# Optimization experiments

Hardware: AMD Instinct MI355X
Metric: run time of the kernel (lower is better)

The kernel has to match this reference:

```python
import jax, jax.numpy as jnp
import numpy as np

T, B, D, H = 512, 64, 1024, 1024


def setup_inputs() -> dict:
    key = jax.random.key(0)
    ks = jax.random.split(key, 8)
    s_ih = 1.0 / np.sqrt(H)
    return {
        "inputs": jax.random.normal(ks[0], (T, B, D), dtype=jnp.float32),
        "h0": jax.random.normal(ks[1], (B, H), dtype=jnp.float32),
        "c0": jax.random.normal(ks[2], (B, H), dtype=jnp.float32),
        "W_ih": jax.random.uniform(ks[3], (4 * H, D), minval=-s_ih, maxval=s_ih, dtype=jnp.float32),
        "W_hh": jax.random.uniform(ks[4], (4 * H, H), minval=-s_ih, maxval=s_ih, dtype=jnp.float32),
        "b_ih": jax.random.uniform(ks[5], (4 * H,), minval=-s_ih, maxval=s_ih, dtype=jnp.float32),
        "b_hh": jax.random.uniform(ks[6], (4 * H,), minval=-s_ih, maxval=s_ih, dtype=jnp.float32),
    }


def _lstm_cell(x, h, c, W_ih, W_hh, b_ih, b_hh):
    # gates: [B, 4H] -> chunks (i, f, g, o), matching torch.nn.LSTMCell
    gates = x @ W_ih.T + b_ih + h @ W_hh.T + b_hh
    i, f, g, o = jnp.split(gates, 4, axis=-1)
    i = jax.nn.sigmoid(i)
    f = jax.nn.sigmoid(f)
    g = jnp.tanh(g)
    o = jax.nn.sigmoid(o)
    c_new = f * c + i * g
    h_new = o * jnp.tanh(c_new)
    return h_new, c_new


def reference(inputs, h0, c0, W_ih, W_hh, b_ih, b_hh):
    def step(carry, x_t):
        h, c = carry
        h, c = _lstm_cell(x_t, h, c, W_ih, W_hh, b_ih, b_hh)
        return (h, c), h

    (h_T, c_T), outputs = jax.lax.scan(step, (h0, c0), inputs)
    # outputs: [T, B, H] stacked per-timestep cell outputs
    return outputs, h_T, c_T
```

## Files before the change

### kernel.cpp

```cpp
#include <hip/hip_runtime.h>

#define T_STEPS 512
#define BATCH   64
#define DIM     1024
#define HID     1024
#define G4      4096
#define KTOT    2048
#define NKS     64

typedef __attribute__((ext_vector_type(8))) short s8v;
typedef __attribute__((ext_vector_type(4))) float f32x4;

__device__ __forceinline__ unsigned short f2bf(float f) {
    unsigned int u = __float_as_uint(f);
    u = u + 0x7FFFu + ((u >> 16) & 1u);
    return (unsigned short)(u >> 16);
}
__device__ __forceinline__ float bf2f(unsigned short s) {
    return __uint_as_float(((unsigned int)s) << 16);
}


__global__ __launch_bounds__(256) void pack_x(
    const float* __restrict__ inp, unsigned short* __restrict__ hi,
    unsigned short* __restrict__ lo)
{
    const size_t tau = (size_t)blockIdx.x * 256 + threadIdx.x;
    const int l  = (int)(tau & 63);
    const int m  = (int)((tau >> 6) & 3);
    const int ks = (int)((tau >> 8) & 31);
    const int t  = (int)(tau >> 13);
    const int b  = 16 * m + (l & 15);
    const int k  = ks * 32 + (l >> 4) * 8;
    const float* src = inp + ((size_t)t * BATCH + b) * DIM + k;
    float f[8];
    *(float4*)&f[0] = *(const float4*)src;
    *(float4*)&f[4] = *(const float4*)(src + 4);
    s8v vh, vl;
#pragma unroll
    for (int e = 0; e < 8; ++e) {
        const unsigned short h8 = f2bf(f[e]);
        vh[e] = (short)h8;
        vl[e] = (short)f2bf(f[e] - bf2f(h8));
    }
    *(s8v*)(hi + tau * 8) = vh;
    *(s8v*)(lo + tau * 8) = vl;
}

__global__ __launch_bounds__(256) void pack_w(
    const float* __restrict__ Wih, const float* __restrict__ Whh,
    unsigned short* __restrict__ hi, unsigned short* __restrict__ lo)
{
    const size_t tau = (size_t)blockIdx.x * 256 + threadIdx.x;
    const int l   = (int)(tau & 63);
    const int ks  = (int)((tau >> 6) & 63);
    const int bid = (int)(tau >> 12);
    const int c   = l & 15;
    const int n   = (c >> 2) * HID + bid * 4 + (c & 3);
    const int k   = ks * 32 + (l >> 4) * 8;
    const float* src = (k < DIM) ? (Wih + (size_t)n * DIM + k)
                                 : (Whh + (size_t)n * HID + (k - DIM));
    float f[8];
    *(float4*)&f[0] = *(const float4*)src;
    *(float4*)&f[4] = *(const float4*)(src + 4);
    s8v vh, vl;
#pragma unroll
    for (int e = 0; e < 8; ++e) {
        const unsigned short h8 = f2bf(f[e]);
        vh[e] = (short)h8;
        vl[e] = (short)f2bf(f[e] - bf2f(h8));
    }
    *(s8v*)(hi + tau * 8) = vh;
    *(s8v*)(lo + tau * 8) = vl;
}

__global__ __launch_bounds__(256) void pack_h0(
    const float* __restrict__ h0, unsigned short* __restrict__ hi,
    unsigned short* __restrict__ lo)
{
    const size_t tau = (size_t)blockIdx.x * 256 + threadIdx.x;
    const int l  = (int)(tau & 63);
    const int m  = (int)((tau >> 6) & 3);
    const int ks = (int)(tau >> 8);
    const int b  = 16 * m + (l & 15);
    const int j  = ks * 32 + (l >> 4) * 8;
    const float* src = h0 + (size_t)b * HID + j;
    float f[8];
    *(float4*)&f[0] = *(const float4*)src;
    *(float4*)&f[4] = *(const float4*)(src + 4);
    s8v vh, vl;
#pragma unroll
    for (int e = 0; e < 8; ++e) {
        const unsigned short h8 = f2bf(f[e]);
        vh[e] = (short)h8;
        vl[e] = (short)f2bf(f[e] - bf2f(h8));
    }
    *(s8v*)(hi + tau * 8) = vh;
    *(s8v*)(lo + tau * 8) = vl;
}

__global__ __launch_bounds__(512) void lstm_step_mfma(
    int t,
    const unsigned short* __restrict__ xPHi, const unsigned short* __restrict__ xPLo,
    const unsigned short* __restrict__ wPHi, const unsigned short* __restrict__ wPLo,
    const unsigned short* __restrict__ hPHi, const unsigned short* __restrict__ hPLo,
    unsigned short* __restrict__ hPHiW,      unsigned short* __restrict__ hPLoW,
    const float* __restrict__ cprev,
    const float* __restrict__ bih, const float* __restrict__ bhh,
    float* __restrict__ cbuf, float* __restrict__ out, float* __restrict__ tailp)
{
    __shared__ float part_s[8][64][8];
    __shared__ float gates_s[64][17];

    const int bid = blockIdx.x;
    const int tid = threadIdx.x;
    const int wv  = __builtin_amdgcn_readfirstlane(tid >> 6);
    const int l   = tid & 63;
    const int mg  = wv >> 2;
    const int kh  = wv & 3;
    const int par = t & 1;
    const int m0  = 2 * mg, m1 = 2 * mg + 1;

    const unsigned short *aHi, *aLo;
    if (kh < 2) {
        const size_t base = (((size_t)t * 32 + kh * 16) * 4) * 512;
        aHi = xPHi + base;  aLo = xPLo + base;
    } else {
        const size_t base = (((size_t)par * 32 + (kh - 2) * 16) * 4) * 512;
        aHi = hPHi + base;  aLo = hPLo + base;
    }
    const unsigned short* bHiP = wPHi + ((size_t)bid * 64 + kh * 16) * 512;
    const unsigned short* bLoP = wPLo + ((size_t)bid * 64 + kh * 16) * 512;

#define LDA(P, i, m) (*(const s8v*)((P) + ((size_t)(i) * 2048 + (m) * 512 + l * 8)))
#define LDB(P, i)    (*(const s8v*)((P) + ((size_t)(i) * 512 + l * 8)))

    f32x4 acc0 = {0.f, 0.f, 0.f, 0.f};
    f32x4 acc1 = {0.f, 0.f, 0.f, 0.f};

    s8v A0h = LDA(aHi, 0, m0), A0l = LDA(aLo, 0, m0);
    s8v A1h = LDA(aHi, 0, m1), A1l = LDA(aLo, 0, m1);
    s8v Bh  = LDB(bHiP, 0),    Bl  = LDB(bLoP, 0);

#pragma unroll 4
    for (int i = 0; i < 16; ++i) {
        s8v nA0h, nA0l, nA1h, nA1l, nBh, nBl;
        if (i < 15) {
            nA0h = LDA(aHi, i + 1, m0); nA0l = LDA(aLo, i + 1, m0);
            nA1h = LDA(aHi, i + 1, m1); nA1l = LDA(aLo, i + 1, m1);
            nBh  = LDB(bHiP, i + 1);    nBl  = LDB(bLoP, i + 1);
        }
        acc0 = __builtin_amdgcn_mfma_f32_16x16x32_bf16(A0h, Bh, acc0, 0, 0, 0);
        acc1 = __builtin_amdgcn_mfma_f32_16x16x32_bf16(A1h, Bh, acc1, 0, 0, 0);
        acc0 = __builtin_amdgcn_mfma_f32_16x16x32_bf16(A0h, Bl, acc0, 0, 0, 0);
        acc1 = __builtin_amdgcn_mfma_f32_16x16x32_bf16(A1h, Bl, acc1, 0, 0, 0);
        acc0 = __builtin_amdgcn_mfma_f32_16x16x32_bf16(A0l, Bh, acc0, 0, 0, 0);
        acc1 = __builtin_amdgcn_mfma_f32_16x16x32_bf16(A1l, Bh, acc1, 0, 0, 0);
        A0h = nA0h; A0l = nA0l; A1h = nA1h; A1l = nA1l; Bh = nBh; Bl = nBl;
    }
#undef LDA
#undef LDB

    *(f32x4*)&part_s[wv][l][0] = acc0;
    *(f32x4*)&part_s[wv][l][4] = acc1;
    __syncthreads();
    if (tid < 128) {
        const int mg2 = tid >> 6, l2 = tid & 63;
        f32x4 s0 = {0.f, 0.f, 0.f, 0.f};
        f32x4 s1 = {0.f, 0.f, 0.f, 0.f};
#pragma unroll
        for (int k = 0; k < 4; ++k) {
            s0 += *(const f32x4*)&part_s[mg2 * 4 + k][l2][0];
            s1 += *(const f32x4*)&part_s[mg2 * 4 + k][l2][4];
        }
        const int c = l2 & 15, rb = (l2 >> 4) * 4;
#pragma unroll
        for (int r = 0; r < 4; ++r) {
            gates_s[16 * (2 * mg2 + 0) + rb + r][c] = s0[r];
            gates_s[16 * (2 * mg2 + 1) + rb + r][c] = s1[r];
        }
    }
    __syncthreads();

    if (tid < 256) {
        const int b  = tid >> 2;
        const int jj = tid & 3;
        const int j  = bid * 4 + jj;
        const float pre_i = gates_s[b][0  + jj] + bih[0 * HID + j] + bhh[0 * HID + j];
        const float pre_f = gates_s[b][4  + jj] + bih[1 * HID + j] + bhh[1 * HID + j];
        const float pre_g = gates_s[b][8  + jj] + bih[2 * HID + j] + bhh[2 * HID + j];
        const float pre_o = gates_s[b][12 + jj] + bih[3 * HID + j] + bhh[3 * HID + j];
        const float ig = 1.0f / (1.0f + __expf(-pre_i));
        const float fg = 1.0f / (1.0f + __expf(-pre_f));
        const float gg = tanhf(pre_g);
        const float og = 1.0f / (1.0f + __expf(-pre_o));
        const float cp = cprev[b * HID + j];
        const float cn = fg * cp + ig * gg;
        const float hn = og * tanhf(cn);
        cbuf[b * HID + j] = cn;
        out[((size_t)t * BATCH + b) * HID + j] = hn;
        if (t == T_STEPS - 1) {
            tailp[b * HID + j] = hn;
            tailp[(size_t)BATCH * HID + b * HID + j] = cn;
        }
        const int parn = par ^ 1;
        const unsigned short hhi = f2bf(hn);
        const unsigned short hlo = f2bf(hn - bf2f(hhi));
        const size_t idx = ((((size_t)parn * 32 + (j >> 5)) * 4 + (b >> 4)) * 64
                            + ((b & 15) + 16 * ((j & 31) >> 3))) * 8 + (j & 7);
        hPHiW[idx] = hhi;
        hPLoW[idx] = hlo;
    }
}

__global__ __launch_bounds__(512) void lstm_step_f32(
    const float* __restrict__ x, const float* __restrict__ hprev,
    const float* __restrict__ cprev,
    const float* __restrict__ Wih, const float* __restrict__ Whh,
    const float* __restrict__ bih, const float* __restrict__ bhh,
    float* __restrict__ cnext, float* __restrict__ hout,
    float* __restrict__ tail)
{
    __shared__ float h_s[8][16][68];
    __shared__ float w_s[8][16][20];
    __shared__ float gates_s[64][17];
    float* part_s = &h_s[0][0][0];

    const int bid = blockIdx.x;
    const int tid = threadIdx.x;
    const int j0  = bid * 4;
    const int wv  = tid >> 6;
    const int gl  = tid & 63;
    const int b0  = (gl >> 2) * 4;
    const int c0_ = (gl & 3) * 4;

    const float* __restrict__ src = (wv < 4) ? x   : hprev;
    const float* __restrict__ W   = (wv < 4) ? Wih : Whh;
    const int kbase = (wv & 3) * 256;

    float acc[4][4] = {};
    float4 hv[4], wvf;

#pragma unroll
    for (int r = 0; r < 4; ++r) {
        const int fidx = r * 64 + gl;
        hv[r] = *(const float4*)(src + (fidx >> 2) * DIM + kbase + (fidx & 3) * 4);
    }
    {
        const int c = gl >> 2, k4 = (gl & 3) * 4;
        const int n = (c >> 2) * HID + j0 + (c & 3);
        wvf = *(const float4*)(W + (size_t)n * DIM + kbase + k4);
    }

    for (int ci = 0; ci < 16; ++ci) {
#pragma unroll
        for (int r = 0; r < 4; ++r) {
            const int fidx = r * 64 + gl;
            const int b = fidx >> 2, k4 = (fidx & 3) * 4;
            h_s[wv][k4 + 0][b] = hv[r].x; h_s[wv][k4 + 1][b] = hv[r].y;
            h_s[wv][k4 + 2][b] = hv[r].z; h_s[wv][k4 + 3][b] = hv[r].w;
        }
        {
            const int c = gl >> 2, k4 = (gl & 3) * 4;
            w_s[wv][k4 + 0][c] = wvf.x; w_s[wv][k4 + 1][c] = wvf.y;
            w_s[wv][k4 + 2][c] = wvf.z; w_s[wv][k4 + 3][c] = wvf.w;
        }
        if (ci < 15) {
            const int kb = kbase + (ci + 1) * 16;
#pragma unroll
            for (int r = 0; r < 4; ++r) {
                const int fidx = r * 64 + gl;
                hv[r] = *(const float4*)(src + (fidx >> 2) * DIM + kb + (fidx & 3) * 4);
            }
            {
                const int c = gl >> 2, k4 = (gl & 3) * 4;
                const int n = (c >> 2) * HID + j0 + (c & 3);
                wvf = *(const float4*)(W + (size_t)n * DIM + kb + k4);
            }
        }
#pragma unroll
        for (int kk = 0; kk < 16; ++kk) {
            const float4 h4 = *(const float4*)&h_s[wv][kk][b0];
            const float4 w4 = *(const float4*)&w_s[wv][kk][c0_];
            const float hr[4] = {h4.x, h4.y, h4.z, h4.w};
            const float wr[4] = {w4.x, w4.y, w4.z, w4.w};
#pragma unroll
            for (int i = 0; i < 4; ++i)
#pragma unroll
                for (int j = 0; j < 4; ++j)
                    acc[i][j] += hr[i] * wr[j];
        }
    }

    __syncthreads();
#pragma unroll
    for (int i = 0; i < 4; ++i)
#pragma unroll
        for (int j = 0; j < 4; ++j)
            part_s[tid * 17 + i * 4 + j] = acc[i][j];
    __syncthreads();
    if (tid < 64) {
#pragma unroll
        for (int i = 0; i < 4; ++i)
#pragma unroll
            for (int j = 0; j < 4; ++j) {
                const int idx = i * 4 + j;
                float s = 0.0f;
#pragma unroll
                for (int p = 0; p < 8; ++p)
                    s += part_s[(gl + 64 * p) * 17 + idx];
                gates_s[b0 + i][c0_ + j] = s;
            }
    }
    __syncthreads();

    if (tid < 256) {
        const int b  = tid >> 2;
        const int jj = tid & 3;
        const int j  = j0 + jj;
        const float pre_i = gates_s[b][0  + jj] + bih[0 * HID + j] + bhh[0 * HID + j];
        const float pre_f = gates_s[b][4  + jj] + bih[1 * HID + j] + bhh[1 * HID + j];
        const float pre_g = gates_s[b][8  + jj] + bih[2 * HID + j] + bhh[2 * HID + j];
        const float pre_o = gates_s[b][12 + jj] + bih[3 * HID + j] + bhh[3 * HID + j];
        const float ig = 1.0f / (1.0f + __expf(-pre_i));
        const float fg = 1.0f / (1.0f + __expf(-pre_f));
        const float gg = tanhf(pre_g);
        const float og = 1.0f / (1.0f + __expf(-pre_o));
        const float cp = cprev[b * HID + j];
        const float cn = fg * cp + ig * gg;
        const float hn = og * tanhf(cn);
        cnext[b * HID + j] = cn;
        hout[b * HID + j]  = hn;
        if (tail) {
            tail[b * HID + j] = hn;
            tail[(size_t)BATCH * HID + b * HID + j] = cn;
        }
    }
}

extern "C" void kernel_launch(void* const* d_in, const int* in_sizes, int n_in,
                              void* d_out, int out_size, void* d_ws, size_t ws_size,
                              hipStream_t stream) {
    const float* inputs = (const float*)d_in[0];
    const float* h0     = (const float*)d_in[1];
    const float* c0     = (const float*)d_in[2];
    const float* W_ih   = (const float*)d_in[3];
    const float* W_hh   = (const float*)d_in[4];
    const float* b_ih   = (const float*)d_in[5];
    const float* b_hh   = (const float*)d_in[6];
    float* out = (float*)d_out;

    const size_t XP = (size_t)T_STEPS * 32 * 4 * 512;
    const size_t WP = (size_t)256 * 64 * 512;
    const size_t HP = (size_t)2 * 32 * 4 * 512;
    const size_t needB = (2 * XP + 2 * WP + 2 * HP) * sizeof(unsigned short)
                         + (size_t)BATCH * HID * sizeof(float);

    if (ws_size >= needB) {
        unsigned short* xPHi = (unsigned short*)d_ws;
        unsigned short* xPLo = xPHi + XP;
        unsigned short* wPHi = xPLo + XP;
        unsigned short* wPLo = wPHi + WP;
        unsigned short* hPHi = wPLo + WP;
        unsigned short* hPLo = hPHi + HP;
        float* cbuf = (float*)(hPLo + HP);

        pack_x<<<dim3(16384), dim3(256), 0, stream>>>(inputs, xPHi, xPLo);
        pack_w<<<dim3(4096),  dim3(256), 0, stream>>>(W_ih, W_hh, wPHi, wPLo);
        pack_h0<<<dim3(32),   dim3(256), 0, stream>>>(h0, hPHi, hPLo);

        for (int t = 0; t < T_STEPS; ++t) {
            const float* cp = (t == 0) ? c0 : cbuf;
            float* tailp = out + (size_t)T_STEPS * BATCH * HID;
            lstm_step_mfma<<<dim3(256), dim3(512), 0, stream>>>(
                t, xPHi, xPLo, wPHi, wPLo, hPHi, hPLo, hPHi, hPLo,
                cp, b_ih, b_hh, cbuf, out, tailp);
        }
    } else {
        float* cbuf = (float*)d_ws;
        for (int t = 0; t < T_STEPS; ++t) {
            const float* x  = inputs + (size_t)t * BATCH * DIM;
            const float* hp = (t == 0) ? h0 : out + (size_t)(t - 1) * BATCH * HID;
            const float* cp = (t == 0) ? c0 : cbuf;
            float* ho   = out + (size_t)t * BATCH * HID;
            float* tailp = (t == T_STEPS - 1)
                         ? out + (size_t)T_STEPS * BATCH * HID : nullptr;
            lstm_step_f32<<<dim3(256), dim3(512), 0, stream>>>(
                x, hp, cp, W_ih, W_hh, b_ih, b_hh, cbuf, ho, tailp);
        }
    }
}
```

Baseline: 7.613 ms.

## Hoist input projection out of recurrence into chunked batched GEMM kernel

Moves the x@W_ih^T part of the gate computation out of the per-step kernel into a separate xproj_chunk kernel. That kernel computes the projection (plus both biases) for 64 timesteps at once and writes the results to a float buffer. The per-step kernel now only reduces over the hidden dimension, halving its serial K-loop, and reads the precomputed projection in its epilogue. The pack_x pre-pass is removed and splitting x into hi/lo bf16 is done inline, at the cost of an extra fp32 buffer round trip and an extra launch per chunk.

```diff
diff --git a/kernel.cpp b/kernel.cpp
--- a/kernel.cpp
+++ b/kernel.cpp
@@ -5,8 +5,7 @@
 #define DIM     1024
 #define HID     1024
 #define G4      4096
-#define KTOT    2048
-#define NKS     64
+#define TCH     64
 
 typedef __attribute__((ext_vector_type(8))) short s8v;
 typedef __attribute__((ext_vector_type(4))) float f32x4;
@@ -20,32 +19,6 @@
     return __uint_as_float(((unsigned int)s) << 16);
 }
 
-
-__global__ __launch_bounds__(256) void pack_x(
-    const float* __restrict__ inp, unsigned short* __restrict__ hi,
-    unsigned short* __restrict__ lo)
-{
-    const size_t tau = (size_t)blockIdx.x * 256 + threadIdx.x;
-    const int l  = (int)(tau & 63);
-    const int m  = (int)((tau >> 6) & 3);
-    const int ks = (int)((tau >> 8) & 31);
-    const int t  = (int)(tau >> 13);
-    const int b  = 16 * m + (l & 15);
-    const int k  = ks * 32 + (l >> 4) * 8;
-    const float* src = inp + ((size_t)t * BATCH + b) * DIM + k;
-    float f[8];
-    *(float4*)&f[0] = *(const float4*)src;
-    *(float4*)&f[4] = *(const float4*)(src + 4);
-    s8v vh, vl;
-#pragma unroll
-    for (int e = 0; e < 8; ++e) {
-        const unsigned short h8 = f2bf(f[e]);
-        vh[e] = (short)h8;
-        vl[e] = (short)f2bf(f[e] - bf2f(h8));
-    }
-    *(s8v*)(hi + tau * 8) = vh;
-    *(s8v*)(lo + tau * 8) = vl;
-}
 
 __global__ __launch_bounds__(256) void pack_w(
     const float* __restrict__ Wih, const float* __restrict__ Whh,
@@ -99,14 +72,99 @@
     *(s8v*)(lo + tau * 8) = vl;
 }
 
+__global__ __launch_bounds__(512) void xproj_chunk(
+    int t0,
+    const float* __restrict__ inp,
+    const unsigned short* __restrict__ wPHi,
+    const unsigned short* __restrict__ wPLo,
+    const float* __restrict__ bih, const float* __restrict__ bhh,
+    float* __restrict__ Xp)
+{
+    const int tid  = threadIdx.x;
+    const int wv   = __builtin_amdgcn_readfirstlane(tid >> 6);
+    const int l    = tid & 63;
+    const int tloc = blockIdx.x >> 6;
+    const int ng   = blockIdx.x & 63;
+    const int t    = t0 + tloc;
+    const int mg   = wv >> 2, nq = wv & 3;
+    const int bid  = ng * 4 + nq;
+    const int m0   = 2 * mg, m1 = m0 + 1;
+
+    const int rowa = l & 15;
+    const int koff = (l >> 4) * 8;
+
+    const float* xbase = inp + (size_t)t * BATCH * DIM;
+    const unsigned short* bHiP = wPHi + ((size_t)bid * 64) * 512;
+    const unsigned short* bLoP = wPLo + ((size_t)bid * 64) * 512;
+
+    f32x4 acc0 = {0.f, 0.f, 0.f, 0.f};
+    f32x4 acc1 = {0.f, 0.f, 0.f, 0.f};
+
+    float4 x0a, x0b, x1a, x1b;
+    s8v Bh, Bl;
+    {
+        const float* p0 = xbase + (16 * m0 + rowa) * DIM + koff;
+        const float* p1 = xbase + (16 * m1 + rowa) * DIM + koff;
+        x0a = *(const float4*)p0; x0b = *(const float4*)(p0 + 4);
+        x1a = *(const float4*)p1; x1b = *(const float4*)(p1 + 4);
+        Bh = *(const s8v*)(bHiP + l * 8);
+        Bl = *(const s8v*)(bLoP + l * 8);
+    }
+
+#pragma unroll 4
+    for (int i = 0; i < 32; ++i) {
+        float f0[8], f1[8];
+        *(float4*)&f0[0] = x0a; *(float4*)&f0[4] = x0b;
+        *(float4*)&f1[0] = x1a; *(float4*)&f1[4] = x1b;
+        s8v A0h, A0l, A1h, A1l;
+#pragma unroll
+        for (int e = 0; e < 8; ++e) {
+            const unsigned short h0e = f2bf(f0[e]);
+            A0h[e] = (short)h0e;
+            A0l[e] = (short)f2bf(f0[e] - bf2f(h0e));
+            const unsigned short h1e = f2bf(f1[e]);
+            A1h[e] = (short)h1e;
+            A1l[e] = (short)f2bf(f1[e] - bf2f(h1e));
+        }
+        float4 n0a, n0b, n1a, n1b; s8v nBh, nBl;
+        if (i < 31) {
+            const int k = (i + 1) * 32 + koff;
+            const float* p0 = xbase + (16 * m0 + rowa) * DIM + k;
+            const float* p1 = xbase + (16 * m1 + rowa) * DIM + k;
+            n0a = *(const float4*)p0; n0b = *(const float4*)(p0 + 4);
+            n1a = *(const float4*)p1; n1b = *(const float4*)(p1 + 4);
+            nBh = *(const s8v*)(bHiP + (size_t)(i + 1) * 512 + l * 8);
+            nBl = *(const s8v*)(bLoP + (size_t)(i + 1) * 512 + l * 8);
+        }
+        acc0 = __builtin_amdgcn_mfma_f32_16x16x32_bf16(A0h, Bh, acc0, 0, 0, 0);
+        acc1 = __builtin_amdgcn_mfma_f32_16x16x32_bf16(A1h, Bh, acc1, 0, 0, 0);
+        acc0 = __builtin_amdgcn_mfma_f32_16x16x32_bf16(A0h, Bl, acc0, 0, 0, 0);
+        acc1 = __builtin_amdgcn_mfma_f32_16x16x32_bf16(A1h, Bl, acc1, 0, 0, 0);
+        acc0 = __builtin_amdgcn_mfma_f32_16x16x32_bf16(A0l, Bh, acc0, 0, 0, 0);
+        acc1 = __builtin_amdgcn_mfma_f32_16x16x32_bf16(A1l, Bh, acc1, 0, 0, 0);
+        x0a = n0a; x0b = n0b; x1a = n1a; x1b = n1b; Bh = nBh; Bl = nBl;
+    }
+
+    const int col = l & 15;
+    const int n   = (col >> 2) * HID + bid * 4 + (col & 3);
+    const float bias = bih[n] + bhh[n];
+    const int tc = t & (TCH - 1);
+    float* op = Xp + (((size_t)tc * 256 + bid) * 64) * 16;
+#pragma unroll
+    for (int r = 0; r < 4; ++r) {
+        const int row = (l >> 4) * 4 + r;
+        op[(16 * m0 + row) * 16 + col] = acc0[r] + bias;
+        op[(16 * m1 + row) * 16 + col] = acc1[r] + bias;
+    }
+}
+
 __global__ __launch_bounds__(512) void lstm_step_mfma(
     int t,
-    const unsigned short* __restrict__ xPHi, const unsigned short* __restrict__ xPLo,
     const unsigned short* __restrict__ wPHi, const unsigned short* __restrict__ wPLo,
     const unsigned short* __restrict__ hPHi, const unsigned short* __restrict__ hPLo,
     unsigned short* __restrict__ hPHiW,      unsigned short* __restrict__ hPLoW,
+    const float* __restrict__ Xp,
     const float* __restrict__ cprev,
-    const float* __restrict__ bih, const float* __restrict__ bhh,
     float* __restrict__ cbuf, float* __restrict__ out, float* __restrict__ tailp)
 {
     __shared__ float part_s[8][64][8];
@@ -117,20 +175,14 @@
     const int wv  = __builtin_amdgcn_readfirstlane(tid >> 6);
     const int l   = tid & 63;
     const int mg  = wv >> 2;
-    const int kh  = wv & 3;
+    const int kq  = wv & 3;
     const int par = t & 1;
     const int m0  = 2 * mg, m1 = 2 * mg + 1;
 
-    const unsigned short *aHi, *aLo;
-    if (kh < 2) {
-        const size_t base = (((size_t)t * 32 + kh * 16) * 4) * 512;
-        aHi = xPHi + base;  aLo = xPLo + base;
-    } else {
-        const size_t base = (((size_t)par * 32 + (kh - 2) * 16) * 4) * 512;
-        aHi = hPHi + base;  aLo = hPLo + base;
-    }
-    const unsigned short* bHiP = wPHi + ((size_t)bid * 64 + kh * 16) * 512;
-    const unsigned short* bLoP = wPLo + ((size_t)bid * 64 + kh * 16) * 512;
+    const unsigned short* aHi = hPHi + ((size_t)par * 32 + kq * 8) * 2048;
+    const unsigned short* aLo = hPLo + ((size_t)par * 32 + kq * 8) * 2048;
+    const unsigned short* bHiP = wPHi + ((size_t)bid * 64 + 32 + kq * 8) * 512;
+    const unsigned short* bLoP = wPLo + ((size_t)bid * 64 + 32 + kq * 8) * 512;
 
 #define LDA(P, i, m) (*(const s8v*)((P) + ((size_t)(i) * 2048 + (m) * 512 + l * 8)))
 #define LDB(P, i)    (*(const s8v*)((P) + ((size_t)(i) * 512 + l * 8)))
@@ -143,9 +195,9 @@
     s8v Bh  = LDB(bHiP, 0),    Bl  = LDB(bLoP, 0);
 
 #pragma unroll 4
-    for (int i = 0; i < 16; ++i) {
+    for (int i = 0; i < 8; ++i) {
         s8v nA0h, nA0l, nA1h, nA1l, nBh, nBl;
-        if (i < 15) {
+        if (i < 7) {
             nA0h = LDA(aHi, i + 1, m0); nA0l = LDA(aLo, i + 1, m0);
             nA1h = LDA(aHi, i + 1, m1); nA1l = LDA(aLo, i + 1, m1);
             nBh  = LDB(bHiP, i + 1);    nBl  = LDB(bLoP, i + 1);
@@ -186,10 +238,12 @@
         const int b  = tid >> 2;
         const int jj = tid & 3;
         const int j  = bid * 4 + jj;
-        const float pre_i = gates_s[b][0  + jj] + bih[0 * HID + j] + bhh[0 * HID + j];
-        const float pre_f = gates_s[b][4  + jj] + bih[1 * HID + j] + bhh[1 * HID + j];
-        const float pre_g = gates_s[b][8  + jj] + bih[2 * HID + j] + bhh[2 * HID + j];
-        const float pre_o = gates_s[b][12 + jj] + bih[3 * HID + j] + bhh[3 * HID + j];
+        const int tc = t & (TCH - 1);
+        const float* xp = Xp + (((size_t)tc * 256 + bid) * 64 + b) * 16;
+        const float pre_i = gates_s[b][0  + jj] + xp[0  + jj];
+        const float pre_f = gates_s[b][4  + jj] + xp[4  + jj];
+        const float pre_g = gates_s[b][8  + jj] + xp[8  + jj];
+        const float pre_o = gates_s[b][12 + jj] + xp[12 + jj];
         const float ig = 1.0f / (1.0f + __expf(-pre_i));
         const float fg = 1.0f / (1.0f + __expf(-pre_f));
         const float gg = tanhf(pre_g);
@@ -350,31 +404,34 @@
     const float* b_hh   = (const float*)d_in[6];
     float* out = (float*)d_out;
 
-    const size_t XP = (size_t)T_STEPS * 32 * 4 * 512;
-    const size_t WP = (size_t)256 * 64 * 512;
-    const size_t HP = (size_t)2 * 32 * 4 * 512;
-    const size_t needB = (2 * XP + 2 * WP + 2 * HP) * sizeof(unsigned short)
-                         + (size_t)BATCH * HID * sizeof(float);
+    const size_t WPn = (size_t)256 * 64 * 512;
+    const size_t HPn = (size_t)2 * 32 * 4 * 512;
+    const size_t XPn = (size_t)TCH * 256 * 64 * 16;
+    const size_t needB = (2 * WPn + 2 * HPn) * sizeof(unsigned short)
+                       + (XPn + (size_t)BATCH * HID) * sizeof(float);
 
     if (ws_size >= needB) {
-        unsigned short* xPHi = (unsigned short*)d_ws;
-        unsigned short* xPLo = xPHi + XP;
-        unsigned short* wPHi = xPLo + XP;
-        unsigned short* wPLo = wPHi + WP;
-        unsigned short* hPHi = wPLo + WP;
-        unsigned short* hPLo = hPHi + HP;
-        float* cbuf = (float*)(hPLo + HP);
-
-        pack_x<<<dim3(16384), dim3(256), 0, stream>>>(inputs, xPHi, xPLo);
-        pack_w<<<dim3(4096),  dim3(256), 0, stream>>>(W_ih, W_hh, wPHi, wPLo);
-        pack_h0<<<dim3(32),   dim3(256), 0, stream>>>(h0, hPHi, hPLo);
-
-        for (int t = 0; t < T_STEPS; ++t) {
-            const float* cp = (t == 0) ? c0 : cbuf;
-            float* tailp = out + (size_t)T_STEPS * BATCH * HID;
-            lstm_step_mfma<<<dim3(256), dim3(512), 0, stream>>>(
-                t, xPHi, xPLo, wPHi, wPLo, hPHi, hPLo, hPHi, hPLo,
-                cp, b_ih, b_hh, cbuf, out, tailp);
+        unsigned short* wPHi = (unsigned short*)d_ws;
+        unsigned short* wPLo = wPHi + WPn;
+        unsigned short* hPHi = wPLo + WPn;
+        unsigned short* hPLo = hPHi + HPn;
+        float* Xp   = (float*)(hPLo + HPn);
+        float* cbuf = Xp + XPn;
+        float* tailp = out + (size_t)T_STEPS * BATCH * HID;
+
+        pack_w<<<dim3(4096), dim3(256), 0, stream>>>(W_ih, W_hh, wPHi, wPLo);
+        pack_h0<<<dim3(32),  dim3(256), 0, stream>>>(h0, hPHi, hPLo);
+
+        for (int c = 0; c < T_STEPS / TCH; ++c) {
+            xproj_chunk<<<dim3(TCH * 64), dim3(512), 0, stream>>>(
+                c * TCH, inputs, wPHi, wPLo, b_ih, b_hh, Xp);
+            for (int tl = 0; tl < TCH; ++tl) {
+                const int t = c * TCH + tl;
+                const float* cp = (t == 0) ? c0 : cbuf;
+                lstm_step_mfma<<<dim3(256), dim3(512), 0, stream>>>(
+                    t, wPHi, wPLo, hPHi, hPLo, hPHi, hPLo,
+                    Xp, cp, cbuf, out, tailp);
+            }
         }
     } else {
         float* cbuf = (float*)d_ws;
@@ -382,7 +439,7 @@
             const float* x  = inputs + (size_t)t * BATCH * DIM;
             const float* hp = (t == 0) ? h0 : out + (size_t)(t - 1) * BATCH * HID;
             const float* cp = (t == 0) ? c0 : cbuf;
-            float* ho   = out + (size_t)t * BATCH * HID;
+            float* ho    = out + (size_t)t * BATCH * HID;
             float* tailp = (t == T_STEPS - 1)
                          ? out + (size_t)T_STEPS * BATCH * HID : nullptr;
             lstm_step_f32<<<dim3(256), dim3(512), 0, stream>>>(
```

After: 8.095 ms. 6.3% more time.

## Replace per-timestep launches with persistent cooperative kernel using grid sync

Applied to the files above, without the earlier changes.

Fuses the 512 per-step kernel launches into one persistent cooperative kernel that loops over time, separating steps with grid.sync(). Cell state stays in shared memory per block and the bias sums are hoisted out of the loop, so the global cbuf round trip and repeated bias loads are removed. The goal is to drop per-step launch overhead. In exchange each step pays a grid-wide barrier, the launch needs all 256 blocks co-resident, and hPHi/hPLo lose __restrict__ because they are read and written in the same kernel.

```diff
diff --git a/kernel.cpp b/kernel.cpp
--- a/kernel.cpp
+++ b/kernel.cpp
@@ -1,12 +1,13 @@
 #include <hip/hip_runtime.h>
+#include <hip/hip_cooperative_groups.h>
+
+namespace cg = cooperative_groups;
 
 #define T_STEPS 512
 #define BATCH   64
 #define DIM     1024
 #define HID     1024
 #define G4      4096
-#define KTOT    2048
-#define NKS     64
 
 typedef __attribute__((ext_vector_type(8))) short s8v;
 typedef __attribute__((ext_vector_type(4))) float f32x4;
@@ -99,18 +100,19 @@
     *(s8v*)(lo + tau * 8) = vl;
 }
 
-__global__ __launch_bounds__(512) void lstm_step_mfma(
-    int t,
+__global__ __launch_bounds__(512) void lstm_persist(
     const unsigned short* __restrict__ xPHi, const unsigned short* __restrict__ xPLo,
     const unsigned short* __restrict__ wPHi, const unsigned short* __restrict__ wPLo,
-    const unsigned short* __restrict__ hPHi, const unsigned short* __restrict__ hPLo,
-    unsigned short* __restrict__ hPHiW,      unsigned short* __restrict__ hPLoW,
-    const float* __restrict__ cprev,
+    unsigned short* hPHi, unsigned short* hPLo,
+    const float* __restrict__ c0,
     const float* __restrict__ bih, const float* __restrict__ bhh,
-    float* __restrict__ cbuf, float* __restrict__ out, float* __restrict__ tailp)
+    float* __restrict__ out, float* __restrict__ tailp)
 {
+    cg::grid_group grid = cg::this_grid();
+
     __shared__ float part_s[8][64][8];
     __shared__ float gates_s[64][17];
+    __shared__ float c_s[64][4];
 
     const int bid = blockIdx.x;
     const int tid = threadIdx.x;
@@ -118,99 +120,115 @@
     const int l   = tid & 63;
     const int mg  = wv >> 2;
     const int kh  = wv & 3;
-    const int par = t & 1;
     const int m0  = 2 * mg, m1 = 2 * mg + 1;
 
-    const unsigned short *aHi, *aLo;
-    if (kh < 2) {
-        const size_t base = (((size_t)t * 32 + kh * 16) * 4) * 512;
-        aHi = xPHi + base;  aLo = xPLo + base;
-    } else {
-        const size_t base = (((size_t)par * 32 + (kh - 2) * 16) * 4) * 512;
-        aHi = hPHi + base;  aLo = hPLo + base;
-    }
-    const unsigned short* bHiP = wPHi + ((size_t)bid * 64 + kh * 16) * 512;
-    const unsigned short* bLoP = wPLo + ((size_t)bid * 64 + kh * 16) * 512;
-
-#define LDA(P, i, m) (*(const s8v*)((P) + ((size_t)(i) * 2048 + (m) * 512 + l * 8)))
-#define LDB(P, i)    (*(const s8v*)((P) + ((size_t)(i) * 512 + l * 8)))
-
-    f32x4 acc0 = {0.f, 0.f, 0.f, 0.f};
-    f32x4 acc1 = {0.f, 0.f, 0.f, 0.f};
-
-    s8v A0h = LDA(aHi, 0, m0), A0l = LDA(aLo, 0, m0);
-    s8v A1h = LDA(aHi, 0, m1), A1l = LDA(aLo, 0, m1);
-    s8v Bh  = LDB(bHiP, 0),    Bl  = LDB(bLoP, 0);
-
-#pragma unroll 4
-    for (int i = 0; i < 16; ++i) {
-        s8v nA0h, nA0l, nA1h, nA1l, nBh, nBl;
-        if (i < 15) {
-            nA0h = LDA(aHi, i + 1, m0); nA0l = LDA(aLo, i + 1, m0);
-            nA1h = LDA(aHi, i + 1, m1); nA1l = LDA(aLo, i + 1, m1);
-            nBh  = LDB(bHiP, i + 1);    nBl  = LDB(bLoP, i + 1);
-        }
-        acc0 = __builtin_amdgcn_mfma_f32_16x16x32_bf16(A0h, Bh, acc0, 0, 0, 0);
-        acc1 = __builtin_amdgcn_mfma_f32_16x16x32_bf16(A1h, Bh, acc1, 0, 0, 0);
-        acc0 = __builtin_amdgcn_mfma_f32_16x16x32_bf16(A0h, Bl, acc0, 0, 0, 0);
-        acc1 = __builtin_amdgcn_mfma_f32_16x16x32_bf16(A1h, Bl, acc1, 0, 0, 0);
-        acc0 = __builtin_amdgcn_mfma_f32_16x16x32_bf16(A0l, Bh, acc0, 0, 0, 0);
-        acc1 = __builtin_amdgcn_mfma_f32_16x16x32_bf16(A1l, Bh, acc1, 0, 0, 0);
-        A0h = nA0h; A0l = nA0l; A1h = nA1h; A1l = nA1l; Bh = nBh; Bl = nBl;
-    }
-#undef LDA
-#undef LDB
-
-    *(f32x4*)&part_s[wv][l][0] = acc0;
-    *(f32x4*)&part_s[wv][l][4] = acc1;
-    __syncthreads();
-    if (tid < 128) {
-        const int mg2 = tid >> 6, l2 = tid & 63;
-        f32x4 s0 = {0.f, 0.f, 0.f, 0.f};
-        f32x4 s1 = {0.f, 0.f, 0.f, 0.f};
-#pragma unroll
-        for (int k = 0; k < 4; ++k) {
-            s0 += *(const f32x4*)&part_s[mg2 * 4 + k][l2][0];
-            s1 += *(const f32x4*)&part_s[mg2 * 4 + k][l2][4];
-        }
-        const int c = l2 & 15, rb = (l2 >> 4) * 4;
-#pragma unroll
-        for (int r = 0; r < 4; ++r) {
-            gates_s[16 * (2 * mg2 + 0) + rb + r][c] = s0[r];
-            gates_s[16 * (2 * mg2 + 1) + rb + r][c] = s1[r];
-        }
-    }
-    __syncthreads();
-
+    float bsum[4];
     if (tid < 256) {
         const int b  = tid >> 2;
         const int jj = tid & 3;
         const int j  = bid * 4 + jj;
-        const float pre_i = gates_s[b][0  + jj] + bih[0 * HID + j] + bhh[0 * HID + j];
-        const float pre_f = gates_s[b][4  + jj] + bih[1 * HID + j] + bhh[1 * HID + j];
-        const float pre_g = gates_s[b][8  + jj] + bih[2 * HID + j] + bhh[2 * HID + j];
-        const float pre_o = gates_s[b][12 + jj] + bih[3 * HID + j] + bhh[3 * HID + j];
-        const float ig = 1.0f / (1.0f + __expf(-pre_i));
-        const float fg = 1.0f / (1.0f + __expf(-pre_f));
-        const float gg = tanhf(pre_g);
-        const float og = 1.0f / (1.0f + __expf(-pre_o));
-        const float cp = cprev[b * HID + j];
-        const float cn = fg * cp + ig * gg;
-        const float hn = og * tanhf(cn);
-        cbuf[b * HID + j] = cn;
-        out[((size_t)t * BATCH + b) * HID + j] = hn;
-        if (t == T_STEPS - 1) {
-            tailp[b * HID + j] = hn;
-            tailp[(size_t)BATCH * HID + b * HID + j] = cn;
-        }
-        const int parn = par ^ 1;
-        const unsigned short hhi = f2bf(hn);
-        const unsigned short hlo = f2bf(hn - bf2f(hhi));
-        const size_t idx = ((((size_t)parn * 32 + (j >> 5)) * 4 + (b >> 4)) * 64
-                            + ((b & 15) + 16 * ((j & 31) >> 3))) * 8 + (j & 7);
-        hPHiW[idx] = hhi;
-        hPLoW[idx] = hlo;
-    }
+        c_s[b][jj] = c0[b * HID + j];
+#pragma unroll
+        for (int g = 0; g < 4; ++g)
+            bsum[g] = bih[g * HID + j] + bhh[g * HID + j];
+    }
+    __syncthreads();
+
+    const unsigned short* bHiP = wPHi + ((size_t)bid * 64 + kh * 16) * 512;
+    const unsigned short* bLoP = wPLo + ((size_t)bid * 64 + kh * 16) * 512;
+
+#define LDA(P, i, m) (*(const s8v*)((P) + ((size_t)(i) * 2048 + (m) * 512 + l * 8)))
+#define LDB(P, i)    (*(const s8v*)((P) + ((size_t)(i) * 512 + l * 8)))
+
+    for (int t = 0; t < T_STEPS; ++t) {
+        const int par = t & 1;
+
+        const unsigned short *aHi, *aLo;
+        if (kh < 2) {
+            const size_t base = (((size_t)t * 32 + kh * 16) * 4) * 512;
+            aHi = xPHi + base;  aLo = xPLo + base;
+        } else {
+            const size_t base = (((size_t)par * 32 + (kh - 2) * 16) * 4) * 512;
+            aHi = hPHi + base;  aLo = hPLo + base;
+        }
+
+        f32x4 acc0 = {0.f, 0.f, 0.f, 0.f};
+        f32x4 acc1 = {0.f, 0.f, 0.f, 0.f};
+
+        s8v A0h = LDA(aHi, 0, m0), A0l = LDA(aLo, 0, m0);
+        s8v A1h = LDA(aHi, 0, m1), A1l = LDA(aLo, 0, m1);
+        s8v Bh  = LDB(bHiP, 0),    Bl  = LDB(bLoP, 0);
+
+#pragma unroll 4
+        for (int i = 0; i < 16; ++i) {
+            s8v nA0h, nA0l, nA1h, nA1l, nBh, nBl;
+            if (i < 15) {
+                nA0h = LDA(aHi, i + 1, m0); nA0l = LDA(aLo, i + 1, m0);
+                nA1h = LDA(aHi, i + 1, m1); nA1l = LDA(aLo, i + 1, m1);
+                nBh  = LDB(bHiP, i + 1);    nBl  = LDB(bLoP, i + 1);
+            }
+            acc0 = __builtin_amdgcn_mfma_f32_16x16x32_bf16(A0h, Bh, acc0, 0, 0, 0);
+            acc1 = __builtin_amdgcn_mfma_f32_16x16x32_bf16(A1h, Bh, acc1, 0, 0, 0);
+            acc0 = __builtin_amdgcn_mfma_f32_16x16x32_bf16(A0h, Bl, acc0, 0, 0, 0);
+            acc1 = __builtin_amdgcn_mfma_f32_16x16x32_bf16(A1h, Bl, acc1, 0, 0, 0);
+            acc0 = __builtin_amdgcn_mfma_f32_16x16x32_bf16(A0l, Bh, acc0, 0, 0, 0);
+            acc1 = __builtin_amdgcn_mfma_f32_16x16x32_bf16(A1l, Bh, acc1, 0, 0, 0);
+            A0h = nA0h; A0l = nA0l; A1h = nA1h; A1l = nA1l; Bh = nBh; Bl = nBl;
+        }
+
+        *(f32x4*)&part_s[wv][l][0] = acc0;
+        *(f32x4*)&part_s[wv][l][4] = acc1;
+        __syncthreads();
+        if (tid < 128) {
+            const int mg2 = tid >> 6, l2 = tid & 63;
+            f32x4 s0 = {0.f, 0.f, 0.f, 0.f};
+            f32x4 s1 = {0.f, 0.f, 0.f, 0.f};
+#pragma unroll
+            for (int k = 0; k < 4; ++k) {
+                s0 += *(const f32x4*)&part_s[mg2 * 4 + k][l2][0];
+                s1 += *(const f32x4*)&part_s[mg2 * 4 + k][l2][4];
+            }
+            const int c = l2 & 15, rb = (l2 >> 4) * 4;
+#pragma unroll
+            for (int r = 0; r < 4; ++r) {
+                gates_s[16 * (2 * mg2 + 0) + rb + r][c] = s0[r];
+                gates_s[16 * (2 * mg2 + 1) + rb + r][c] = s1[r];
+            }
+        }
+        __syncthreads();
+
+        if (tid < 256) {
+            const int b  = tid >> 2;
+            const int jj = tid & 3;
+            const int j  = bid * 4 + jj;
+            const float pre_i = gates_s[b][0  + jj] + bsum[0];
+            const float pre_f = gates_s[b][4  + jj] + bsum[1];
+            const float pre_g = gates_s[b][8  + jj] + bsum[2];
+            const float pre_o = gates_s[b][12 + jj] + bsum[3];
+            const float ig = 1.0f / (1.0f + __expf(-pre_i));
+            const float fg = 1.0f / (1.0f + __expf(-pre_f));
+            const float gg = tanhf(pre_g);
+            const float og = 1.0f / (1.0f + __expf(-pre_o));
+            const float cn = fg * c_s[b][jj] + ig * gg;
+            const float hn = og * tanhf(cn);
+            c_s[b][jj] = cn;
+            out[((size_t)t * BATCH + b) * HID + j] = hn;
+            if (t == T_STEPS - 1) {
+                tailp[b * HID + j] = hn;
+                tailp[(size_t)BATCH * HID + b * HID + j] = cn;
+            }
+            const int parn = par ^ 1;
+            const unsigned short hhi = f2bf(hn);
+            const unsigned short hlo = f2bf(hn - bf2f(hhi));
+            const size_t idx = ((((size_t)parn * 32 + (j >> 5)) * 4 + (b >> 4)) * 64
+                                + ((b & 15) + 16 * ((j & 31) >> 3))) * 8 + (j & 7);
+            hPHi[idx] = hhi;
+            hPLo[idx] = hlo;
+        }
+        grid.sync();
+    }
+#undef LDA
+#undef LDB
 }
 
 __global__ __launch_bounds__(512) void lstm_step_f32(
@@ -354,7 +372,7 @@
     const size_t WP = (size_t)256 * 64 * 512;
     const size_t HP = (size_t)2 * 32 * 4 * 512;
     const size_t needB = (2 * XP + 2 * WP + 2 * HP) * sizeof(unsigned short)
-                         + (size_t)BATCH * HID * sizeof(float);
+                       + (size_t)BATCH * HID * sizeof(float);
 
     if (ws_size >= needB) {
         unsigned short* xPHi = (unsigned short*)d_ws;
@@ -363,26 +381,24 @@
         unsigned short* wPLo = wPHi + WP;
         unsigned short* hPHi = wPLo + WP;
         unsigned short* hPLo = hPHi + HP;
-        float* cbuf = (float*)(hPLo + HP);
+        float* tailp = out + (size_t)T_STEPS * BATCH * HID;
 
         pack_x<<<dim3(16384), dim3(256), 0, stream>>>(inputs, xPHi, xPLo);
         pack_w<<<dim3(4096),  dim3(256), 0, stream>>>(W_ih, W_hh, wPHi, wPLo);
         pack_h0<<<dim3(32),   dim3(256), 0, stream>>>(h0, hPHi, hPLo);
 
-        for (int t = 0; t < T_STEPS; ++t) {
-            const float* cp = (t == 0) ? c0 : cbuf;
-            float* tailp = out + (size_t)T_STEPS * BATCH * HID;
-            lstm_step_mfma<<<dim3(256), dim3(512), 0, stream>>>(
-                t, xPHi, xPLo, wPHi, wPLo, hPHi, hPLo, hPHi, hPLo,
-                cp, b_ih, b_hh, cbuf, out, tailp);
-        }
+        void* args[] = {(void*)&xPHi, (void*)&xPLo, (void*)&wPHi, (void*)&wPLo,
+                        (void*)&hPHi, (void*)&hPLo, (void*)&c0,
+                        (void*)&b_ih, (void*)&b_hh, (void*)&out, (void*)&tailp};
+        hipLaunchCooperativeKernel((void*)lstm_persist, dim3(256), dim3(512),
+                                   args, 0, stream);
     } else {
         float* cbuf = (float*)d_ws;
         for (int t = 0; t < T_STEPS; ++t) {
             const float* x  = inputs + (size_t)t * BATCH * DIM;
             const float* hp = (t == 0) ? h0 : out + (size_t)(t - 1) * BATCH * HID;
             const float* cp = (t == 0) ? c0 : cbuf;
-            float* ho   = out + (size_t)t * BATCH * HID;
+            float* ho    = out + (size_t)t * BATCH * HID;
             float* tailp = (t == T_STEPS - 1)
                          ? out + (size_t)T_STEPS * BATCH * HID : nullptr;
             lstm_step_f32<<<dim3(256), dim3(512), 0, stream>>>(
```

New measurement: 21.66 ms. 185% more time.
